# Optimization experiments

Measured on AMD Instinct MI355X. Metric: run time of the kernel, lower is better.

Reference implementation:

```python
import jax, jax.numpy as jnp
import numpy as np

NO_FEATURES = 512
NO_HEADS = 8
HEAD_DIM = NO_FEATURES // NO_HEADS


def setup_inputs() -> dict:
    key = jax.random.key(0)
    ks = jax.random.split(key, 10)
    B, S, D = 4, 2048, NO_FEATURES
    s = 1.0 / np.sqrt(D)
    return {
        "x": jax.random.normal(ks[0], (B, S, D), dtype=jnp.float32),
        "ln_gamma": jnp.ones((D,), jnp.float32),
        "ln_beta": jnp.zeros((D,), jnp.float32),
        "Wq": jax.random.uniform(ks[1], (D, D), jnp.float32, -s, s),
        "bq": jax.random.uniform(ks[2], (D,), jnp.float32, -s, s),
        "Wk": jax.random.uniform(ks[3], (D, D), jnp.float32, -s, s),
        "bk": jax.random.uniform(ks[4], (D,), jnp.float32, -s, s),
        "Wv": jax.random.uniform(ks[5], (D, D), jnp.float32, -s, s),
        "bv": jax.random.uniform(ks[6], (D,), jnp.float32, -s, s),
        "Wo": jax.random.uniform(ks[7], (D, D), jnp.float32, -s, s),
        "bo": jax.random.uniform(ks[8], (D,), jnp.float32, -s, s),
    }


def reference(x, ln_gamma, ln_beta, Wq, bq, Wk, bk, Wv, bv, Wo, bo):
    B, S, D = x.shape
    H, Dh = NO_HEADS, D // NO_HEADS
    # Pre-LayerNorm (eps = 1e-5, torch default)
    mu = jnp.mean(x, axis=-1, keepdims=True)
    var = jnp.mean(jnp.square(x - mu), axis=-1, keepdims=True)
    xn = (x - mu) * jax.lax.rsqrt(var + 1e-5) * ln_gamma + ln_beta
    # QKV projections (torch Linear: x @ W.T + b)
    q = (xn @ Wq.T + bq).reshape(B, S, H, Dh).transpose(0, 2, 1, 3)
    k = (xn @ Wk.T + bk).reshape(B, S, H, Dh).transpose(0, 2, 1, 3)
    v = (xn @ Wv.T + bv).reshape(B, S, H, Dh).transpose(0, 2, 1, 3)
    scale = Dh ** -0.5
    scores = jnp.einsum("bhqd,bhkd->bhqk", q, k) * scale  # [B,H,S,S]
    attn = jax.nn.softmax(scores, axis=-1)
    # dropout is identity in eval mode
    out = jnp.einsum("bhqk,bhkd->bhqd", attn, v)
    out = out.transpose(0, 2, 1, 3).reshape(B, S, D)
    return out @ Wo.T + bo
```

## Files before the change

kernel.cpp:

```cpp
#include <hip/hip_runtime.h>
#include <cstdint>
#include <cstddef>

#define NB 4
#define NS 2048
#define ND 512
#define NH 8
#define DH 64
#define MTOK (NB*NS)

typedef __bf16 bf16x8 __attribute__((ext_vector_type(8)));
typedef float f32x4 __attribute__((ext_vector_type(4)));
typedef float f32x16 __attribute__((ext_vector_type(16)));
typedef unsigned int u32x4 __attribute__((ext_vector_type(4)));
typedef unsigned short ushort_t;
typedef unsigned int uint_t;

__device__ __forceinline__ unsigned short f2bf(float f) {
  unsigned int u = __builtin_bit_cast(unsigned int, f);
  return (unsigned short)((u + 0x7fffu + ((u >> 16) & 1u)) >> 16);
}

__device__ __forceinline__ uint_t cvtpk(float lo, float hi) {
  uint_t r;
  asm("v_cvt_pk_bf16_f32 %0, %1, %2" : "=v"(r) : "v"(lo), "v"(hi));
  return r;
}

__device__ __forceinline__ void pswap(uint_t &a, uint_t &b) {
  asm("v_permlane32_swap_b32 %0, %1" : "+v"(a), "+v"(b));
}

__device__ __forceinline__ void gload_lds16(const void* g, void* l) {
  __builtin_amdgcn_global_load_lds(
      (const __attribute__((address_space(1))) unsigned int*)g,
      (__attribute__((address_space(3))) unsigned int*)l,
      16, 0, 0);
}

__device__ __forceinline__ bf16x8 ld8(const ushort_t* p) { return *(const bf16x8*)p; }

__global__ __launch_bounds__(256) void ln_kernel(
    const float* __restrict__ x, const float* __restrict__ gamma,
    const float* __restrict__ beta, ushort_t* __restrict__ xn)
{
  const int row  = blockIdx.x * 4 + (threadIdx.x >> 6);
  const int lane = threadIdx.x & 63;
  const float4* xr = (const float4*)(x + (size_t)row * ND);
  float4 a = xr[lane*2], b = xr[lane*2+1];
  float v[8] = {a.x,a.y,a.z,a.w,b.x,b.y,b.z,b.w};
  float s = 0.f, s2 = 0.f;
#pragma unroll
  for (int j = 0; j < 8; ++j) { s += v[j]; s2 += v[j]*v[j]; }
#pragma unroll
  for (int mk = 1; mk < 64; mk <<= 1) { s += __shfl_xor(s, mk); s2 += __shfl_xor(s2, mk); }
  const float mu = s * (1.0f/ND);
  const float rs = rsqrtf(s2*(1.0f/ND) - mu*mu + 1e-5f);
  const float4* g4 = (const float4*)gamma;
  const float4* b4 = (const float4*)beta;
  float4 g0 = g4[lane*2], g1 = g4[lane*2+1];
  float4 e0 = b4[lane*2], e1 = b4[lane*2+1];
  float gv[8] = {g0.x,g0.y,g0.z,g0.w,g1.x,g1.y,g1.z,g1.w};
  float ev[8] = {e0.x,e0.y,e0.z,e0.w,e1.x,e1.y,e1.z,e1.w};
  unsigned short o[8];
#pragma unroll
  for (int j = 0; j < 8; ++j) o[j] = f2bf((v[j]-mu)*rs*gv[j] + ev[j]);
  uint4 ov;
  ov.x = (uint_t)o[0] | ((uint_t)o[1]<<16);
  ov.y = (uint_t)o[2] | ((uint_t)o[3]<<16);
  ov.z = (uint_t)o[4] | ((uint_t)o[5]<<16);
  ov.w = (uint_t)o[6] | ((uint_t)o[7]<<16);
  ((uint4*)(xn + (size_t)row*ND))[lane] = ov;
}

__global__ __launch_bounds__(256) void convert_w(
    const float* __restrict__ Wq, const float* __restrict__ Wk,
    const float* __restrict__ Wv, const float* __restrict__ Wo,
    ushort_t* __restrict__ wqkv, ushort_t* __restrict__ wob)
{
  const int t = blockIdx.x*256 + threadIdx.x;
  const int i = t*8;
  const float* src; ushort_t* dst;
  if (i < 1536*512) {
    const int n = i >> 9, c = i & 511;
    const float* W = (n < 512) ? Wq : (n < 1024) ? Wk : Wv;
    src = W + ((size_t)(n & 511) << 9) + c;
    dst = wqkv + i;
  } else {
    const int jj = i - 1536*512;
    src = Wo + jj; dst = wob + jj;
  }
  float4 a = ((const float4*)src)[0], b = ((const float4*)src)[1];
  uint4 o;
  o.x = (uint_t)f2bf(a.x) | ((uint_t)f2bf(a.y)<<16);
  o.y = (uint_t)f2bf(a.z) | ((uint_t)f2bf(a.w)<<16);
  o.z = (uint_t)f2bf(b.x) | ((uint_t)f2bf(b.y)<<16);
  o.w = (uint_t)f2bf(b.z) | ((uint_t)f2bf(b.w)<<16);
  *(uint4*)dst = o;
}

template<int EPI>
__global__ __launch_bounds__(256, 2) void gemm_bt(
    const ushort_t* __restrict__ A, const ushort_t* __restrict__ Bw, int Kd,
    const float* __restrict__ bq, const float* __restrict__ bk, const float* __restrict__ bv,
    ushort_t* __restrict__ qa, ushort_t* __restrict__ ka, ushort_t* __restrict__ vta,
    const float* __restrict__ bo, float* __restrict__ outp)
{
  __shared__ ushort_t lA[2][128*32];
  __shared__ ushort_t lB[2][128*32];
  const int tid = threadIdx.x;
  const int wave = tid >> 6, lane = tid & 63;
  const int m0 = blockIdx.y * 128, n0 = blockIdx.x * 128;
  const int wr = (wave >> 1) * 64, wc = (wave & 1) * 64;

  f32x4 acc[4][4] = {};

  const ushort_t* aS = A  + (size_t)(m0 + tid/4) * Kd + (tid & 3) * 8;
  const ushort_t* bS = Bw + (size_t)(n0 + tid/4) * Kd + (tid & 3) * 8;
  const size_t half = (size_t)64 * Kd;
  const int NT = Kd / 32;

#define STAGE(BUF, K0)                                            \
  gload_lds16(aS + (K0),        lA[BUF] + wave*512);              \
  gload_lds16(aS + half + (K0), lA[BUF] + 2048 + wave*512);       \
  gload_lds16(bS + (K0),        lB[BUF] + wave*512);              \
  gload_lds16(bS + half + (K0), lB[BUF] + 2048 + wave*512);

  STAGE(0, 0);
  int cur = 0;
  for (int t = 0; t < NT; ++t) {
    if (t + 1 < NT) {
      STAGE(cur ^ 1, (t + 1) * 32);
      asm volatile("s_waitcnt vmcnt(4)" ::: "memory");
    } else {
      asm volatile("s_waitcnt vmcnt(0)" ::: "memory");
    }
    __builtin_amdgcn_s_barrier();
    asm volatile("" ::: "memory");
    bf16x8 af[4], bfr[4];
#pragma unroll
    for (int i = 0; i < 4; ++i)
      af[i] = *(const bf16x8*)(lA[cur] + (wr + i*16 + (lane&15))*32 + (lane>>4)*8);
#pragma unroll
    for (int j = 0; j < 4; ++j)
      bfr[j] = *(const bf16x8*)(lB[cur] + (wc + j*16 + (lane&15))*32 + (lane>>4)*8);
#pragma unroll
    for (int i = 0; i < 4; ++i)
#pragma unroll
      for (int j = 0; j < 4; ++j)
        acc[i][j] = __builtin_amdgcn_mfma_f32_16x16x32_bf16(af[i], bfr[j], acc[i][j], 0, 0, 0);
    asm volatile("s_waitcnt lgkmcnt(0)" ::: "memory");
    __builtin_amdgcn_s_barrier();
    asm volatile("" ::: "memory");
    cur ^= 1;
  }
#undef STAGE

  if (EPI == 0) {
    const float QSCALE = 0.18033688011112042f;
#pragma unroll
    for (int j = 0; j < 4; ++j) {
      const int n = n0 + wc + j*16 + (lane & 15);
      const int which = n >> 9;
      const int nn = n & 511;
      const int h = nn >> 6, d = nn & 63;
      const float bb = (which == 0) ? bq[nn] : (which == 1) ? bk[nn] : bv[nn];
#pragma unroll
      for (int i = 0; i < 4; ++i)
#pragma unroll
        for (int r = 0; r < 4; ++r) {
          const int mm = m0 + wr + i*16 + 4*(lane>>4) + r;
          const int b = mm >> 11, s = mm & 2047;
          const int bh = b*NH + h;
          const float av = acc[i][j][r] + bb;
          if (which == 0) {
            qa[(((size_t)bh*64 + (s>>5))*4 + (d>>4))*512
               + (((d>>3)&1)*32 + (s&31))*8 + (d&7)] = f2bf(av * QSCALE);
          } else if (which == 1) {
            ka[(((size_t)bh*64 + (s>>5))*4 + (d>>4))*512
               + (((d>>3)&1)*32 + (s&31))*8 + (d&7)] = f2bf(av);
          } else {
            vta[(((size_t)bh*128 + (s>>4))*2 + (d>>5))*512
               + (((s>>3)&1)*32 + (d&31))*8 + (s&7)] = f2bf(av);
          }
        }
    }
  } else {
#pragma unroll
    for (int j = 0; j < 4; ++j) {
      const int n = n0 + wc + j*16 + (lane & 15);
      const float bb = bo[n];
#pragma unroll
      for (int i = 0; i < 4; ++i)
#pragma unroll
        for (int r = 0; r < 4; ++r) {
          const int m = m0 + wr + i*16 + 4*(lane>>4) + r;
          outp[(size_t)m*ND + n] = acc[i][j][r] + bb;
        }
    }
  }
}

__global__ __launch_bounds__(256) void attn_kernel(
    const ushort_t* __restrict__ qfv, const ushort_t* __restrict__ kfv,
    const ushort_t* __restrict__ vfv, ushort_t* __restrict__ ao)
{
  const int blk  = blockIdx.x;
  const int bh   = (blk & 7) | ((blk >> 7) << 3);
  const int qblk = (blk >> 3) & 15;
  const int w    = threadIdx.x >> 6;
  const int lane = threadIdx.x & 63;
  const int lo5 = lane & 31, hi = lane >> 5;
  const int qt = qblk*4 + w;

  const ushort_t* qb = qfv + (((size_t)bh*64 + qt)*4)*512 + lane*8;
  bf16x8 qf[4];
#pragma unroll
  for (int s = 0; s < 4; ++s) qf[s] = ld8(qb + s*512);

  const ushort_t* kb = kfv + ((size_t)bh*256)*512 + lane*8;
  const ushort_t* vb = vfv + ((size_t)bh*256)*512 + lane*8;

  f32x16 o0 = {}, o1 = {};
  f32x16 lsv = {};
  const f32x16 FZ = {};

  bf16x8 kf0[4], kf1[4];
#pragma unroll
  for (int s = 0; s < 4; ++s) {
    kf0[s] = ld8(kb + (size_t)s*512);
    kf1[s] = ld8(kb + (size_t)(4+s)*512);
  }

  for (int j0 = 0; j0 < NS; j0 += 64) {
    bf16x8 vf0[4], vf1[4];
    const int kv16 = j0 >> 4;
#pragma unroll
    for (int ks = 0; ks < 4; ++ks) {
      vf0[ks] = ld8(vb + ((size_t)(kv16+ks)*2    )*512);
      vf1[ks] = ld8(vb + ((size_t)(kv16+ks)*2 + 1)*512);
    }
    f32x16 s0, s1;
    __builtin_amdgcn_s_setprio(1);
    s0 = __builtin_amdgcn_mfma_f32_32x32x16_bf16(kf0[0], qf[0], FZ, 0, 0, 0);
    s1 = __builtin_amdgcn_mfma_f32_32x32x16_bf16(kf1[0], qf[0], FZ, 0, 0, 0);
#pragma unroll
    for (int s = 1; s < 4; ++s) {
      s0 = __builtin_amdgcn_mfma_f32_32x32x16_bf16(kf0[s], qf[s], s0, 0, 0, 0);
      s1 = __builtin_amdgcn_mfma_f32_32x32x16_bf16(kf1[s], qf[s], s1, 0, 0, 0);
    }
    __builtin_amdgcn_s_setprio(0);
    if (j0 + 64 < NS) {
      const int kt = (j0 >> 5) + 2;
#pragma unroll
      for (int s = 0; s < 4; ++s) {
        kf0[s] = ld8(kb + ((size_t)(kt  )*4 + s)*512);
        kf1[s] = ld8(kb + ((size_t)(kt+1)*4 + s)*512);
      }
    }
#pragma unroll
    for (int r = 0; r < 16; ++r) s0[r] = __builtin_amdgcn_exp2f(s0[r]);
    lsv += s0;
#pragma unroll
    for (int r = 0; r < 16; ++r) s1[r] = __builtin_amdgcn_exp2f(s1[r]);
    lsv += s1;
    bf16x8 pf[4];
    {
      uint_t a, b, c, d;
      a = cvtpk(s0[0],  s0[1]);  b = cvtpk(s0[4],  s0[5]);  pswap(a, b);
      c = cvtpk(s0[2],  s0[3]);  d = cvtpk(s0[6],  s0[7]);  pswap(c, d);
      pf[0] = __builtin_bit_cast(bf16x8, (u32x4){a, c, b, d});
      a = cvtpk(s0[8],  s0[9]);  b = cvtpk(s0[12], s0[13]); pswap(a, b);
      c = cvtpk(s0[10], s0[11]); d = cvtpk(s0[14], s0[15]); pswap(c, d);
      pf[1] = __builtin_bit_cast(bf16x8, (u32x4){a, c, b, d});
      a = cvtpk(s1[0],  s1[1]);  b = cvtpk(s1[4],  s1[5]);  pswap(a, b);
      c = cvtpk(s1[2],  s1[3]);  d = cvtpk(s1[6],  s1[7]);  pswap(c, d);
      pf[2] = __builtin_bit_cast(bf16x8, (u32x4){a, c, b, d});
      a = cvtpk(s1[8],  s1[9]);  b = cvtpk(s1[12], s1[13]); pswap(a, b);
      c = cvtpk(s1[10], s1[11]); d = cvtpk(s1[14], s1[15]); pswap(c, d);
      pf[3] = __builtin_bit_cast(bf16x8, (u32x4){a, c, b, d});
    }
    __builtin_amdgcn_s_setprio(1);
#pragma unroll
    for (int ks = 0; ks < 4; ++ks) {
      o0 = __builtin_amdgcn_mfma_f32_32x32x16_bf16(vf0[ks], pf[ks], o0, 0, 0, 0);
      o1 = __builtin_amdgcn_mfma_f32_32x32x16_bf16(vf1[ks], pf[ks], o1, 0, 0, 0);
    }
    __builtin_amdgcn_s_setprio(0);
  }

  float l = 0.f;
#pragma unroll
  for (int r = 0; r < 16; ++r) l += lsv[r];
  l += __shfl_xor(l, 32);
  const float rl = __builtin_amdgcn_rcpf(l);
  const int b = bh >> 3, h = bh & 7;
  const int srow = qt*32 + lo5;
  ushort_t* ob = ao + ((size_t)(b*NS + srow))*ND + h*DH;
#pragma unroll
  for (int dt = 0; dt < 2; ++dt) {
    f32x16& oo = dt ? o1 : o0;
#pragma unroll
    for (int r = 0; r < 16; r += 2) {
      const int d = (r & 3) + 8*(r >> 2) + 4*hi + dt*32;
      *(uint_t*)(ob + d) = cvtpk(oo[r]*rl, oo[r+1]*rl);
    }
  }
}

extern "C" void kernel_launch(void* const* d_in, const int* in_sizes, int n_in,
                              void* d_out, int out_size, void* d_ws, size_t ws_size,
                              hipStream_t stream)
{
  const float* x  = (const float*)d_in[0];
  const float* g  = (const float*)d_in[1];
  const float* be = (const float*)d_in[2];
  const float* Wq = (const float*)d_in[3];
  const float* bq = (const float*)d_in[4];
  const float* Wk = (const float*)d_in[5];
  const float* bk = (const float*)d_in[6];
  const float* Wv = (const float*)d_in[7];
  const float* bv = (const float*)d_in[8];
  const float* Wo = (const float*)d_in[9];
  const float* bo = (const float*)d_in[10];
  float* out = (float*)d_out;

  char* w = (char*)d_ws;
  ushort_t* xn   = (ushort_t*)w; w += (size_t)MTOK*ND*2;
  ushort_t* wqkv = (ushort_t*)w; w += (size_t)1536*512*2;
  ushort_t* wob  = (ushort_t*)w; w += (size_t)512*512*2;
  ushort_t* qa   = (ushort_t*)w; w += (size_t)MTOK*ND*2;
  ushort_t* ka   = (ushort_t*)w; w += (size_t)MTOK*ND*2;
  ushort_t* vta  = (ushort_t*)w; w += (size_t)MTOK*ND*2;
  ushort_t* ao   = (ushort_t*)w; w += (size_t)MTOK*ND*2;

  ln_kernel<<<MTOK/4, 256, 0, stream>>>(x, g, be, xn);
  convert_w<<<512, 256, 0, stream>>>(Wq, Wk, Wv, Wo, wqkv, wob);
  gemm_bt<0><<<dim3(12, 64), 256, 0, stream>>>(xn, wqkv, ND,
      bq, bk, bv, qa, ka, vta, nullptr, nullptr);
  attn_kernel<<<512, 256, 0, stream>>>(qa, ka, vta, ao);
  gemm_bt<1><<<dim3(4, 64), 256, 0, stream>>>(ao, wob, ND,
      nullptr, nullptr, nullptr, nullptr, nullptr, nullptr, bo, out);
}
```

Measured before the change: 103.1 us.

## Process two query tiles per wave in attention to reuse K/V fragments

Each wave now handles two 32-row query tiles, so every K and V fragment loaded from global memory feeds twice as many MFMAs. The grid shrinks from 512 to 256 blocks. The two tiles' softmax and PV work are split by a sched_barrier so that one tile's exp work can overlap the other's MFMAs. The setprio hints are removed and row sums use four partial accumulators. The cost is more registers and half as many blocks, which on a 256-CU part means about one block per CU and weaker latency hiding.

```diff
diff --git a/kernel.cpp b/kernel.cpp
--- a/kernel.cpp
+++ b/kernel.cpp
@@ -206,24 +206,26 @@
     const ushort_t* __restrict__ vfv, ushort_t* __restrict__ ao)
 {
   const int blk  = blockIdx.x;
-  const int bh   = (blk & 7) | ((blk >> 7) << 3);
-  const int qblk = (blk >> 3) & 15;
+  const int bh   = (blk & 7) | ((blk >> 6) << 3);
+  const int qblk = (blk >> 3) & 7;
   const int w    = threadIdx.x >> 6;
   const int lane = threadIdx.x & 63;
   const int lo5 = lane & 31, hi = lane >> 5;
-  const int qt = qblk*4 + w;
-
-  const ushort_t* qb = qfv + (((size_t)bh*64 + qt)*4)*512 + lane*8;
-  bf16x8 qf[4];
-#pragma unroll
-  for (int s = 0; s < 4; ++s) qf[s] = ld8(qb + s*512);
+  const int qtA = qblk*8 + w*2;
+  const int qtB = qtA + 1;
+
+  const ushort_t* qbA = qfv + (((size_t)bh*64 + qtA)*4)*512 + lane*8;
+  const ushort_t* qbB = qfv + (((size_t)bh*64 + qtB)*4)*512 + lane*8;
+  bf16x8 qfA[4], qfB[4];
+#pragma unroll
+  for (int s = 0; s < 4; ++s) { qfA[s] = ld8(qbA + s*512); qfB[s] = ld8(qbB + s*512); }
 
   const ushort_t* kb = kfv + ((size_t)bh*256)*512 + lane*8;
   const ushort_t* vb = vfv + ((size_t)bh*256)*512 + lane*8;
 
-  f32x16 o0 = {}, o1 = {};
-  f32x16 lsv = {};
-  const f32x16 FZ = {};
+  f32x16 oA0 = {}, oA1 = {}, oB0 = {}, oB1 = {};
+  float lA0 = 0.f, lA1 = 0.f, lA2 = 0.f, lA3 = 0.f;
+  float lB0 = 0.f, lB1 = 0.f, lB2 = 0.f, lB3 = 0.f;
 
   bf16x8 kf0[4], kf1[4];
 #pragma unroll
@@ -240,70 +242,134 @@
       vf0[ks] = ld8(vb + ((size_t)(kv16+ks)*2    )*512);
       vf1[ks] = ld8(vb + ((size_t)(kv16+ks)*2 + 1)*512);
     }
-    f32x16 s0, s1;
-    __builtin_amdgcn_s_setprio(1);
-    s0 = __builtin_amdgcn_mfma_f32_32x32x16_bf16(kf0[0], qf[0], FZ, 0, 0, 0);
-    s1 = __builtin_amdgcn_mfma_f32_32x32x16_bf16(kf1[0], qf[0], FZ, 0, 0, 0);
-#pragma unroll
-    for (int s = 1; s < 4; ++s) {
-      s0 = __builtin_amdgcn_mfma_f32_32x32x16_bf16(kf0[s], qf[s], s0, 0, 0, 0);
-      s1 = __builtin_amdgcn_mfma_f32_32x32x16_bf16(kf1[s], qf[s], s1, 0, 0, 0);
-    }
-    __builtin_amdgcn_s_setprio(0);
-    if (j0 + 64 < NS) {
-      const int kt = (j0 >> 5) + 2;
+    {
+      f32x16 s0 = {}, s1 = {};
 #pragma unroll
       for (int s = 0; s < 4; ++s) {
-        kf0[s] = ld8(kb + ((size_t)(kt  )*4 + s)*512);
-        kf1[s] = ld8(kb + ((size_t)(kt+1)*4 + s)*512);
-      }
-    }
-#pragma unroll
-    for (int r = 0; r < 16; ++r) s0[r] = __builtin_amdgcn_exp2f(s0[r]);
-    lsv += s0;
-#pragma unroll
-    for (int r = 0; r < 16; ++r) s1[r] = __builtin_amdgcn_exp2f(s1[r]);
-    lsv += s1;
-    bf16x8 pf[4];
+        s0 = __builtin_amdgcn_mfma_f32_32x32x16_bf16(kf0[s], qfA[s], s0, 0, 0, 0);
+        s1 = __builtin_amdgcn_mfma_f32_32x32x16_bf16(kf1[s], qfA[s], s1, 0, 0, 0);
+      }
+#pragma unroll
+      for (int r = 0; r < 16; r += 4) {
+        s0[r]   = __builtin_amdgcn_exp2f(s0[r]);   lA0 += s0[r];
+        s0[r+1] = __builtin_amdgcn_exp2f(s0[r+1]); lA1 += s0[r+1];
+        s0[r+2] = __builtin_amdgcn_exp2f(s0[r+2]); lA2 += s0[r+2];
+        s0[r+3] = __builtin_amdgcn_exp2f(s0[r+3]); lA3 += s0[r+3];
+      }
+#pragma unroll
+      for (int r = 0; r < 16; r += 4) {
+        s1[r]   = __builtin_amdgcn_exp2f(s1[r]);   lA0 += s1[r];
+        s1[r+1] = __builtin_amdgcn_exp2f(s1[r+1]); lA1 += s1[r+1];
+        s1[r+2] = __builtin_amdgcn_exp2f(s1[r+2]); lA2 += s1[r+2];
+        s1[r+3] = __builtin_amdgcn_exp2f(s1[r+3]); lA3 += s1[r+3];
+      }
+      bf16x8 pf[4];
+      {
+        uint_t a, b, c, d;
+        a = cvtpk(s0[0],  s0[1]);  b = cvtpk(s0[4],  s0[5]);  pswap(a, b);
+        c = cvtpk(s0[2],  s0[3]);  d = cvtpk(s0[6],  s0[7]);  pswap(c, d);
+        pf[0] = __builtin_bit_cast(bf16x8, (u32x4){a, c, b, d});
+        a = cvtpk(s0[8],  s0[9]);  b = cvtpk(s0[12], s0[13]); pswap(a, b);
+        c = cvtpk(s0[10], s0[11]); d = cvtpk(s0[14], s0[15]); pswap(c, d);
+        pf[1] = __builtin_bit_cast(bf16x8, (u32x4){a, c, b, d});
+        a = cvtpk(s1[0],  s1[1]);  b = cvtpk(s1[4],  s1[5]);  pswap(a, b);
+        c = cvtpk(s1[2],  s1[3]);  d = cvtpk(s1[6],  s1[7]);  pswap(c, d);
+        pf[2] = __builtin_bit_cast(bf16x8, (u32x4){a, c, b, d});
+        a = cvtpk(s1[8],  s1[9]);  b = cvtpk(s1[12], s1[13]); pswap(a, b);
+        c = cvtpk(s1[10], s1[11]); d = cvtpk(s1[14], s1[15]); pswap(c, d);
+        pf[3] = __builtin_bit_cast(bf16x8, (u32x4){a, c, b, d});
+      }
+#pragma unroll
+      for (int ks = 0; ks < 4; ++ks) {
+        oA0 = __builtin_amdgcn_mfma_f32_32x32x16_bf16(vf0[ks], pf[ks], oA0, 0, 0, 0);
+        oA1 = __builtin_amdgcn_mfma_f32_32x32x16_bf16(vf1[ks], pf[ks], oA1, 0, 0, 0);
+      }
+    }
+    __builtin_amdgcn_sched_barrier(0);
     {
-      uint_t a, b, c, d;
-      a = cvtpk(s0[0],  s0[1]);  b = cvtpk(s0[4],  s0[5]);  pswap(a, b);
-      c = cvtpk(s0[2],  s0[3]);  d = cvtpk(s0[6],  s0[7]);  pswap(c, d);
-      pf[0] = __builtin_bit_cast(bf16x8, (u32x4){a, c, b, d});
-      a = cvtpk(s0[8],  s0[9]);  b = cvtpk(s0[12], s0[13]); pswap(a, b);
-      c = cvtpk(s0[10], s0[11]); d = cvtpk(s0[14], s0[15]); pswap(c, d);
-      pf[1] = __builtin_bit_cast(bf16x8, (u32x4){a, c, b, d});
-      a = cvtpk(s1[0],  s1[1]);  b = cvtpk(s1[4],  s1[5]);  pswap(a, b);
-      c = cvtpk(s1[2],  s1[3]);  d = cvtpk(s1[6],  s1[7]);  pswap(c, d);
-      pf[2] = __builtin_bit_cast(bf16x8, (u32x4){a, c, b, d});
-      a = cvtpk(s1[8],  s1[9]);  b = cvtpk(s1[12], s1[13]); pswap(a, b);
-      c = cvtpk(s1[10], s1[11]); d = cvtpk(s1[14], s1[15]); pswap(c, d);
-      pf[3] = __builtin_bit_cast(bf16x8, (u32x4){a, c, b, d});
-    }
-    __builtin_amdgcn_s_setprio(1);
-#pragma unroll
-    for (int ks = 0; ks < 4; ++ks) {
-      o0 = __builtin_amdgcn_mfma_f32_32x32x16_bf16(vf0[ks], pf[ks], o0, 0, 0, 0);
-      o1 = __builtin_amdgcn_mfma_f32_32x32x16_bf16(vf1[ks], pf[ks], o1, 0, 0, 0);
-    }
-    __builtin_amdgcn_s_setprio(0);
-  }
-
-  float l = 0.f;
-#pragma unroll
-  for (int r = 0; r < 16; ++r) l += lsv[r];
-  l += __shfl_xor(l, 32);
-  const float rl = __builtin_amdgcn_rcpf(l);
+      f32x16 s0 = {}, s1 = {};
+#pragma unroll
+      for (int s = 0; s < 4; ++s) {
+        s0 = __builtin_amdgcn_mfma_f32_32x32x16_bf16(kf0[s], qfB[s], s0, 0, 0, 0);
+        s1 = __builtin_amdgcn_mfma_f32_32x32x16_bf16(kf1[s], qfB[s], s1, 0, 0, 0);
+      }
+      if (j0 + 64 < NS) {
+        const int kt = (j0 >> 5) + 2;
+#pragma unroll
+        for (int s = 0; s < 4; ++s) {
+          kf0[s] = ld8(kb + ((size_t)(kt  )*4 + s)*512);
+          kf1[s] = ld8(kb + ((size_t)(kt+1)*4 + s)*512);
+        }
+      }
+#pragma unroll
+      for (int r = 0; r < 16; r += 4) {
+        s0[r]   = __builtin_amdgcn_exp2f(s0[r]);   lB0 += s0[r];
+        s0[r+1] = __builtin_amdgcn_exp2f(s0[r+1]); lB1 += s0[r+1];
+        s0[r+2] = __builtin_amdgcn_exp2f(s0[r+2]); lB2 += s0[r+2];
+        s0[r+3] = __builtin_amdgcn_exp2f(s0[r+3]); lB3 += s0[r+3];
+      }
+#pragma unroll
+      for (int r = 0; r < 16; r += 4) {
+        s1[r]   = __builtin_amdgcn_exp2f(s1[r]);   lB0 += s1[r];
+        s1[r+1] = __builtin_amdgcn_exp2f(s1[r+1]); lB1 += s1[r+1];
+        s1[r+2] = __builtin_amdgcn_exp2f(s1[r+2]); lB2 += s1[r+2];
+        s1[r+3] = __builtin_amdgcn_exp2f(s1[r+3]); lB3 += s1[r+3];
+      }
+      bf16x8 pf[4];
+      {
+        uint_t a, b, c, d;
+        a = cvtpk(s0[0],  s0[1]);  b = cvtpk(s0[4],  s0[5]);  pswap(a, b);
+        c = cvtpk(s0[2],  s0[3]);  d = cvtpk(s0[6],  s0[7]);  pswap(c, d);
+        pf[0] = __builtin_bit_cast(bf16x8, (u32x4){a, c, b, d});
+        a = cvtpk(s0[8],  s0[9]);  b = cvtpk(s0[12], s0[13]); pswap(a, b);
+        c = cvtpk(s0[10], s0[11]); d = cvtpk(s0[14], s0[15]); pswap(c, d);
+        pf[1] = __builtin_bit_cast(bf16x8, (u32x4){a, c, b, d});
+        a = cvtpk(s1[0],  s1[1]);  b = cvtpk(s1[4],  s1[5]);  pswap(a, b);
+        c = cvtpk(s1[2],  s1[3]);  d = cvtpk(s1[6],  s1[7]);  pswap(c, d);
+        pf[2] = __builtin_bit_cast(bf16x8, (u32x4){a, c, b, d});
+        a = cvtpk(s1[8],  s1[9]);  b = cvtpk(s1[12], s1[13]); pswap(a, b);
+        c = cvtpk(s1[10], s1[11]); d = cvtpk(s1[14], s1[15]); pswap(c, d);
+        pf[3] = __builtin_bit_cast(bf16x8, (u32x4){a, c, b, d});
+      }
+#pragma unroll
+      for (int ks = 0; ks < 4; ++ks) {
+        oB0 = __builtin_amdgcn_mfma_f32_32x32x16_bf16(vf0[ks], pf[ks], oB0, 0, 0, 0);
+        oB1 = __builtin_amdgcn_mfma_f32_32x32x16_bf16(vf1[ks], pf[ks], oB1, 0, 0, 0);
+      }
+    }
+  }
+
   const int b = bh >> 3, h = bh & 7;
-  const int srow = qt*32 + lo5;
-  ushort_t* ob = ao + ((size_t)(b*NS + srow))*ND + h*DH;
-#pragma unroll
-  for (int dt = 0; dt < 2; ++dt) {
-    f32x16& oo = dt ? o1 : o0;
-#pragma unroll
-    for (int r = 0; r < 16; r += 2) {
-      const int d = (r & 3) + 8*(r >> 2) + 4*hi + dt*32;
-      *(uint_t*)(ob + d) = cvtpk(oo[r]*rl, oo[r+1]*rl);
+  {
+    float l = (lA0 + lA1) + (lA2 + lA3);
+    l += __shfl_xor(l, 32);
+    const float rl = __builtin_amdgcn_rcpf(l);
+    const int srow = qtA*32 + lo5;
+    ushort_t* ob = ao + ((size_t)(b*NS + srow))*ND + h*DH;
+#pragma unroll
+    for (int dt = 0; dt < 2; ++dt) {
+      f32x16& oo = dt ? oA1 : oA0;
+#pragma unroll
+      for (int r = 0; r < 16; r += 2) {
+        const int d = (r & 3) + 8*(r >> 2) + 4*hi + dt*32;
+        *(uint_t*)(ob + d) = cvtpk(oo[r]*rl, oo[r+1]*rl);
+      }
+    }
+  }
+  {
+    float l = (lB0 + lB1) + (lB2 + lB3);
+    l += __shfl_xor(l, 32);
+    const float rl = __builtin_amdgcn_rcpf(l);
+    const int srow = qtB*32 + lo5;
+    ushort_t* ob = ao + ((size_t)(b*NS + srow))*ND + h*DH;
+#pragma unroll
+    for (int dt = 0; dt < 2; ++dt) {
+      f32x16& oo = dt ? oB1 : oB0;
+#pragma unroll
+      for (int r = 0; r < 16; r += 2) {
+        const int d = (r & 3) + 8*(r >> 2) + 4*hi + dt*32;
+        *(uint_t*)(ob + d) = cvtpk(oo[r]*rl, oo[r+1]*rl);
+      }
     }
   }
 }
@@ -338,7 +404,7 @@
   convert_w<<<512, 256, 0, stream>>>(Wq, Wk, Wv, Wo, wqkv, wob);
   gemm_bt<0><<<dim3(12, 64), 256, 0, stream>>>(xn, wqkv, ND,
       bq, bk, bv, qa, ka, vta, nullptr, nullptr);
-  attn_kernel<<<512, 256, 0, stream>>>(qa, ka, vta, ao);
+  attn_kernel<<<256, 256, 0, stream>>>(qa, ka, vta, ao);
   gemm_bt<1><<<dim3(4, 64), 256, 0, stream>>>(ao, wob, ND,
       nullptr, nullptr, nullptr, nullptr, nullptr, nullptr, bo, out);
 }
```

Result: faster. 98.86 us (-4.1%).

## Merge LN and weight conversion kernels; compute softmax denominator via MFMA

Applied to the files above, without the earlier changes.

Folds the weight-conversion kernel into the LayerNorm launch as extra blocks, removing one kernel launch. In attention, the softmax row sum is now produced by an extra MFMA against an all-ones bf16 operand, replacing the per-iteration vector adds and the final reduction plus cross-lane shuffle. The K/V pointer arithmetic is simplified to incrementing base pointers, and the s_setprio hints are dropped. The denominator now sums the bf16-rounded probabilities, and the extra MFMAs add matrix-unit work per tile.

```diff
diff --git a/kernel.cpp b/kernel.cpp
--- a/kernel.cpp
+++ b/kernel.cpp
@@ -40,10 +40,35 @@
 
 __device__ __forceinline__ bf16x8 ld8(const ushort_t* p) { return *(const bf16x8*)p; }
 
-__global__ __launch_bounds__(256) void ln_kernel(
+__global__ __launch_bounds__(256) void ln_conv(
     const float* __restrict__ x, const float* __restrict__ gamma,
-    const float* __restrict__ beta, ushort_t* __restrict__ xn)
+    const float* __restrict__ beta, ushort_t* __restrict__ xn,
+    const float* __restrict__ Wq, const float* __restrict__ Wk,
+    const float* __restrict__ Wv, const float* __restrict__ Wo,
+    ushort_t* __restrict__ wqkv, ushort_t* __restrict__ wob)
 {
+  if (blockIdx.x >= 2048) {
+    const int t = (blockIdx.x - 2048)*256 + threadIdx.x;
+    const int i = t*8;
+    const float* src; ushort_t* dst;
+    if (i < 1536*512) {
+      const int n = i >> 9, c = i & 511;
+      const float* W = (n < 512) ? Wq : (n < 1024) ? Wk : Wv;
+      src = W + ((size_t)(n & 511) << 9) + c;
+      dst = wqkv + i;
+    } else {
+      const int jj = i - 1536*512;
+      src = Wo + jj; dst = wob + jj;
+    }
+    float4 a = ((const float4*)src)[0], b = ((const float4*)src)[1];
+    uint4 o;
+    o.x = (uint_t)f2bf(a.x) | ((uint_t)f2bf(a.y)<<16);
+    o.y = (uint_t)f2bf(a.z) | ((uint_t)f2bf(a.w)<<16);
+    o.z = (uint_t)f2bf(b.x) | ((uint_t)f2bf(b.y)<<16);
+    o.w = (uint_t)f2bf(b.z) | ((uint_t)f2bf(b.w)<<16);
+    *(uint4*)dst = o;
+    return;
+  }
   const int row  = blockIdx.x * 4 + (threadIdx.x >> 6);
   const int lane = threadIdx.x & 63;
   const float4* xr = (const float4*)(x + (size_t)row * ND);
@@ -71,32 +96,6 @@
   ov.z = (uint_t)o[4] | ((uint_t)o[5]<<16);
   ov.w = (uint_t)o[6] | ((uint_t)o[7]<<16);
   ((uint4*)(xn + (size_t)row*ND))[lane] = ov;
-}
-
-__global__ __launch_bounds__(256) void convert_w(
-    const float* __restrict__ Wq, const float* __restrict__ Wk,
-    const float* __restrict__ Wv, const float* __restrict__ Wo,
-    ushort_t* __restrict__ wqkv, ushort_t* __restrict__ wob)
-{
-  const int t = blockIdx.x*256 + threadIdx.x;
-  const int i = t*8;
-  const float* src; ushort_t* dst;
-  if (i < 1536*512) {
-    const int n = i >> 9, c = i & 511;
-    const float* W = (n < 512) ? Wq : (n < 1024) ? Wk : Wv;
-    src = W + ((size_t)(n & 511) << 9) + c;
-    dst = wqkv + i;
-  } else {
-    const int jj = i - 1536*512;
-    src = Wo + jj; dst = wob + jj;
-  }
-  float4 a = ((const float4*)src)[0], b = ((const float4*)src)[1];
-  uint4 o;
-  o.x = (uint_t)f2bf(a.x) | ((uint_t)f2bf(a.y)<<16);
-  o.y = (uint_t)f2bf(a.z) | ((uint_t)f2bf(a.w)<<16);
-  o.z = (uint_t)f2bf(b.x) | ((uint_t)f2bf(b.y)<<16);
-  o.w = (uint_t)f2bf(b.z) | ((uint_t)f2bf(b.w)<<16);
-  *(uint4*)dst = o;
 }
 
 template<int EPI>
@@ -218,52 +217,49 @@
 #pragma unroll
   for (int s = 0; s < 4; ++s) qf[s] = ld8(qb + s*512);
 
-  const ushort_t* kb = kfv + ((size_t)bh*256)*512 + lane*8;
-  const ushort_t* vb = vfv + ((size_t)bh*256)*512 + lane*8;
-
-  f32x16 o0 = {}, o1 = {};
-  f32x16 lsv = {};
-  const f32x16 FZ = {};
+  const ushort_t* kpA = kfv + ((size_t)bh*256)*512 + lane*8;
+  const ushort_t* kpB = kpA + 2048;
+  const ushort_t* vpA = vfv + ((size_t)bh*256)*512 + lane*8;
+  const ushort_t* vpB = vpA + 2048;
+
+  const uint_t one2 = 0x3F803F80u;
+  const bf16x8 ones = __builtin_bit_cast(bf16x8, (u32x4){one2, one2, one2, one2});
+
+  f32x16 o0 = {}, o1 = {}, ol = {};
 
   bf16x8 kf0[4], kf1[4];
 #pragma unroll
   for (int s = 0; s < 4; ++s) {
-    kf0[s] = ld8(kb + (size_t)s*512);
-    kf1[s] = ld8(kb + (size_t)(4+s)*512);
-  }
-
-  for (int j0 = 0; j0 < NS; j0 += 64) {
+    kf0[s] = ld8(kpA + s*512);
+    kf1[s] = ld8(kpB + s*512);
+  }
+  kpA += 4096; kpB += 4096;
+
+  for (int t = 0; t < 32; ++t) {
     bf16x8 vf0[4], vf1[4];
-    const int kv16 = j0 >> 4;
-#pragma unroll
-    for (int ks = 0; ks < 4; ++ks) {
-      vf0[ks] = ld8(vb + ((size_t)(kv16+ks)*2    )*512);
-      vf1[ks] = ld8(vb + ((size_t)(kv16+ks)*2 + 1)*512);
-    }
-    f32x16 s0, s1;
-    __builtin_amdgcn_s_setprio(1);
-    s0 = __builtin_amdgcn_mfma_f32_32x32x16_bf16(kf0[0], qf[0], FZ, 0, 0, 0);
-    s1 = __builtin_amdgcn_mfma_f32_32x32x16_bf16(kf1[0], qf[0], FZ, 0, 0, 0);
-#pragma unroll
-    for (int s = 1; s < 4; ++s) {
+    vf0[0] = ld8(vpA);        vf1[0] = ld8(vpA + 512);
+    vf0[1] = ld8(vpA + 1024); vf1[1] = ld8(vpA + 1536);
+    vf0[2] = ld8(vpB);        vf1[2] = ld8(vpB + 512);
+    vf0[3] = ld8(vpB + 1024); vf1[3] = ld8(vpB + 1536);
+    vpA += 4096; vpB += 4096;
+    f32x16 s0 = {}, s1 = {};
+#pragma unroll
+    for (int s = 0; s < 4; ++s) {
       s0 = __builtin_amdgcn_mfma_f32_32x32x16_bf16(kf0[s], qf[s], s0, 0, 0, 0);
       s1 = __builtin_amdgcn_mfma_f32_32x32x16_bf16(kf1[s], qf[s], s1, 0, 0, 0);
     }
-    __builtin_amdgcn_s_setprio(0);
-    if (j0 + 64 < NS) {
-      const int kt = (j0 >> 5) + 2;
+    if (t < 31) {
 #pragma unroll
       for (int s = 0; s < 4; ++s) {
-        kf0[s] = ld8(kb + ((size_t)(kt  )*4 + s)*512);
-        kf1[s] = ld8(kb + ((size_t)(kt+1)*4 + s)*512);
+        kf0[s] = ld8(kpA + s*512);
+        kf1[s] = ld8(kpB + s*512);
       }
+      kpA += 4096; kpB += 4096;
     }
 #pragma unroll
     for (int r = 0; r < 16; ++r) s0[r] = __builtin_amdgcn_exp2f(s0[r]);
-    lsv += s0;
 #pragma unroll
     for (int r = 0; r < 16; ++r) s1[r] = __builtin_amdgcn_exp2f(s1[r]);
-    lsv += s1;
     bf16x8 pf[4];
     {
       uint_t a, b, c, d;
@@ -280,20 +276,17 @@
       c = cvtpk(s1[10], s1[11]); d = cvtpk(s1[14], s1[15]); pswap(c, d);
       pf[3] = __builtin_bit_cast(bf16x8, (u32x4){a, c, b, d});
     }
-    __builtin_amdgcn_s_setprio(1);
+#pragma unroll
+    for (int ks = 0; ks < 4; ++ks)
+      ol = __builtin_amdgcn_mfma_f32_32x32x16_bf16(ones, pf[ks], ol, 0, 0, 0);
 #pragma unroll
     for (int ks = 0; ks < 4; ++ks) {
       o0 = __builtin_amdgcn_mfma_f32_32x32x16_bf16(vf0[ks], pf[ks], o0, 0, 0, 0);
       o1 = __builtin_amdgcn_mfma_f32_32x32x16_bf16(vf1[ks], pf[ks], o1, 0, 0, 0);
     }
-    __builtin_amdgcn_s_setprio(0);
-  }
-
-  float l = 0.f;
-#pragma unroll
-  for (int r = 0; r < 16; ++r) l += lsv[r];
-  l += __shfl_xor(l, 32);
-  const float rl = __builtin_amdgcn_rcpf(l);
+  }
+
+  const float rl = __builtin_amdgcn_rcpf(ol[0]);
   const int b = bh >> 3, h = bh & 7;
   const int srow = qt*32 + lo5;
   ushort_t* ob = ao + ((size_t)(b*NS + srow))*ND + h*DH;
@@ -334,8 +327,7 @@
   ushort_t* vta  = (ushort_t*)w; w += (size_t)MTOK*ND*2;
   ushort_t* ao   = (ushort_t*)w; w += (size_t)MTOK*ND*2;
 
-  ln_kernel<<<MTOK/4, 256, 0, stream>>>(x, g, be, xn);
-  convert_w<<<512, 256, 0, stream>>>(Wq, Wk, Wv, Wo, wqkv, wob);
+  ln_conv<<<2560, 256, 0, stream>>>(x, g, be, xn, Wq, Wk, Wv, Wo, wqkv, wob);
   gemm_bt<0><<<dim3(12, 64), 256, 0, stream>>>(xn, wqkv, ND,
       bq, bk, bv, qa, ka, vta, nullptr, nullptr);
   attn_kernel<<<512, 256, 0, stream>>>(qa, ka, vta, ao);
```

After: 104.4 us. About the same (+1.3%).
